# Kernel optimization log

Measured on AMD Instinct MI355X. Metric: run time of the kernel, lower is better.

Reference implementation:

```python
import jax, jax.numpy as jnp
import numpy as np

HEADS = 4
W1 = 7
W2 = 5

def _ln_channel(x, g, b):
    # x: [B,C,H,W]; LayerNorm over channel dim (permute to channel-last)
    xt = x.transpose(0, 2, 3, 1)
    mu = xt.mean(-1, keepdims=True)
    var = xt.var(-1, keepdims=True)
    xt = (xt - mu) / jnp.sqrt(var + 1e-5) * g + b
    return xt.transpose(0, 3, 1, 2)

def _neighborhood_attention(x, qkv_w, qkv_b, proj_w, proj_b, rpb, heads, w):
    # x: [B,C,H,W]; clamped sliding-window (NAT) attention with rel-pos bias
    B, C, H, Wd = x.shape
    hd = C // heads
    xl = x.transpose(0, 2, 3, 1)                      # [B,H,W,C]
    qkv = xl @ qkv_w.T + qkv_b                        # [B,H,W,3C]
    qkv = qkv.reshape(B, H, Wd, 3, heads, hd)
    q = qkv[:, :, :, 0].transpose(0, 3, 1, 2, 4)      # [B,h,H,W,d]
    k = qkv[:, :, :, 1].transpose(0, 3, 1, 2, 4)
    v = qkv[:, :, :, 2].transpose(0, 3, 1, 2, 4)
    q = q * (hd ** -0.5)
    # clamped neighborhood start per row/col
    si = jnp.clip(jnp.arange(H) - w // 2, 0, H - w)   # [H]
    sj = jnp.clip(jnp.arange(Wd) - w // 2, 0, Wd - w) # [W]
    idx_i = si[:, None] + jnp.arange(w)[None, :]      # [H,w]
    idx_j = sj[:, None] + jnp.arange(w)[None, :]      # [W,w]
    # gather neighbor keys/values: [B,h,H,W,w,w,d]
    k_nb = k[:, :, idx_i[:, None, :, None], idx_j[None, :, None, :], :]
    v_nb = v[:, :, idx_i[:, None, :, None], idx_j[None, :, None, :], :]
    attn = jnp.einsum('bnijd,bnijkld->bnijkl', q, k_nb)  # [B,h,H,W,w,w]
    # relative position bias: rel = (w-1) + neighbor_offset - query_offset
    pi = jnp.arange(H) - si                            # [H] in [0,w-1]
    pj = jnp.arange(Wd) - sj
    bi = (w - 1) + jnp.arange(w)[None, :] - pi[:, None]  # [H,w]
    bj = (w - 1) + jnp.arange(w)[None, :] - pj[:, None]  # [W,w]
    bias = rpb[:, bi[:, None, :, None], bj[None, :, None, :]]  # [h,H,W,w,w]
    attn = attn + bias[None]
    attn = jax.nn.softmax(attn.reshape(B, heads, H, Wd, w * w), axis=-1)
    attn = attn.reshape(B, heads, H, Wd, w, w)
    out = jnp.einsum('bnijkl,bnijkld->bnijd', attn, v_nb)  # [B,h,H,W,d]
    out = out.transpose(0, 2, 3, 1, 4).reshape(B, H, Wd, C)
    out = out @ proj_w.T + proj_b
    return out.transpose(0, 3, 1, 2)                   # [B,C,H,W]

def setup_inputs() -> dict:
    key = jax.random.key(0)
    ks = jax.random.split(key, 12)
    B, C, H, W = 2, 128, 56, 56
    s = 0.02
    return {
        'x': jax.random.normal(ks[0], (B, C, H, W), jnp.float32),
        'ln1_g': jnp.ones((C,), jnp.float32),
        'ln1_b': jnp.zeros((C,), jnp.float32),
        'qkv_w1': jax.random.normal(ks[1], (3 * C, C), jnp.float32) * s,
        'qkv_b1': jnp.zeros((3 * C,), jnp.float32),
        'proj_w1': jax.random.normal(ks[2], (C, C), jnp.float32) * s,
        'proj_b1': jnp.zeros((C,), jnp.float32),
        'rpb1': jax.random.normal(ks[3], (HEADS, 2 * W1 - 1, 2 * W1 - 1), jnp.float32) * s,
        'qkv_w2': jax.random.normal(ks[4], (3 * C, C), jnp.float32) * s,
        'qkv_b2': jnp.zeros((3 * C,), jnp.float32),
        'proj_w2': jax.random.normal(ks[5], (C, C), jnp.float32) * s,
        'proj_b2': jnp.zeros((C,), jnp.float32),
        'rpb2': jax.random.normal(ks[6], (HEADS, 2 * W2 - 1, 2 * W2 - 1), jnp.float32) * s,
        'ln2_g': jnp.ones((C,), jnp.float32),
        'ln2_b': jnp.zeros((C,), jnp.float32),
        'fc1_w': jax.random.normal(ks[7], (2 * C, C), jnp.float32) * s,
        'fc1_b': jnp.zeros((2 * C,), jnp.float32),
        'fc2_w': jax.random.normal(ks[8], (C, 2 * C), jnp.float32) * s,
        'fc2_b': jnp.zeros((C,), jnp.float32),
    }

def reference(x, ln1_g, ln1_b, qkv_w1, qkv_b1, proj_w1, proj_b1, rpb1,
              qkv_w2, qkv_b2, proj_w2, proj_b2, rpb2,
              ln2_g, ln2_b, fc1_w, fc1_b, fc2_w, fc2_b):
    xn = _ln_channel(x, ln1_g, ln1_b)
    a = (_neighborhood_attention(xn, qkv_w1, qkv_b1, proj_w1, proj_b1, rpb1, HEADS, W1)
         + _neighborhood_attention(xn, qkv_w2, qkv_b2, proj_w2, proj_b2, rpb2, HEADS, W2))
    x = x + a
    xn2 = _ln_channel(x, ln2_g, ln2_b)
    h = jnp.einsum('bchw,oc->bohw', xn2, fc1_w) + fc1_b[None, :, None, None]
    h = jax.nn.gelu(h, approximate=False)  # torch nn.GELU default = exact erf
    y = jnp.einsum('bchw,oc->bohw', h, fc2_w) + fc2_b[None, :, None, None]
    return x + y
```

## Files before the change

kernel.cpp:

```cpp
#include <hip/hip_runtime.h>
#include <hip/hip_bf16.h>

#define BATCH 2
#define CH    128
#define HH    56
#define WW    56
#define HWS   3136
#define NPOS  6272
#define HEADS 4
#define HD    32

using f32x4 = __attribute__((ext_vector_type(4))) float;
using s16x8 = __attribute__((ext_vector_type(8))) short;

__device__ __forceinline__ unsigned short f2bf(float f) {
  unsigned u = __builtin_bit_cast(unsigned, f);
  u += 0x7FFFu + ((u >> 16) & 1u);
  return (unsigned short)(u >> 16);
}
__device__ __forceinline__ unsigned pack2bf(float a, float b) {
  return (unsigned)f2bf(a) | ((unsigned)f2bf(b) << 16);
}

__global__ __launch_bounds__(256) void convert_weights(
    const float* __restrict__ qw1, const float* __restrict__ qw2,
    const float* __restrict__ pw1, const float* __restrict__ pw2,
    const float* __restrict__ f1w, const float* __restrict__ f2w,
    unsigned short* __restrict__ wb) {
  int bid = blockIdx.x;
  const float* src; unsigned short* dst; int base;
  if (bid < 48)       { src = qw1; dst = wb;           base = bid * 1024; }
  else if (bid < 96)  { src = qw2; dst = wb + 49152;   base = (bid - 48) * 1024; }
  else if (bid < 112) { src = pw1; dst = wb + 98304;   base = (bid - 96) * 1024; }
  else if (bid < 128) { src = pw2; dst = wb + 114688;  base = (bid - 112) * 1024; }
  else if (bid < 160) { src = f1w; dst = wb + 131072;  base = (bid - 128) * 1024; }
  else                { src = f2w; dst = wb + 163840;  base = (bid - 160) * 1024; }
  int i = base + threadIdx.x * 4;
  float4 v = *reinterpret_cast<const float4*>(src + i);
  uint2 o;
  o.x = pack2bf(v.x, v.y);
  o.y = pack2bf(v.z, v.w);
  *reinterpret_cast<uint2*>(dst + i) = o;
}

__global__ __launch_bounds__(256) void ln1_kernel(const float* __restrict__ x,
                                                  const float* __restrict__ g,
                                                  const float* __restrict__ be,
                                                  unsigned short* __restrict__ out) {
  __shared__ float tile[128 * 65];
  __shared__ float mu_s[64];
  __shared__ float rs_s[64];
  const int p0 = blockIdx.x * 64;
  const int b  = (p0 >= HWS) ? 1 : 0;
  const int s0 = p0 - b * HWS;
  const int tid = threadIdx.x;

  for (int idx = tid; idx < 8192; idx += 256) {
    int c = idx >> 6, p = idx & 63;
    tile[c * 65 + p] = x[(size_t)(b * CH + c) * HWS + s0 + p];
  }
  __syncthreads();
  {
    int p = tid >> 2, q = tid & 3;
    float sum = 0.f, sq = 0.f;
#pragma unroll
    for (int t = 0; t < 32; ++t) {
      float v = tile[(q * 32 + t) * 65 + p];
      sum += v; sq += v * v;
    }
    sum += __shfl_xor(sum, 1); sq += __shfl_xor(sq, 1);
    sum += __shfl_xor(sum, 2); sq += __shfl_xor(sq, 2);
    float mu  = sum * 0.0078125f;
    float var = sq * 0.0078125f - mu * mu;
    float rs  = rsqrtf(var + 1e-5f);
    if (q == 0) { mu_s[p] = mu; rs_s[p] = rs; }
  }
  __syncthreads();
  for (int idx = tid; idx < 4096; idx += 256) {
    int nl = idx >> 6, c2 = idx & 63;
    int c0 = 2 * c2;
    float v0 = (tile[c0 * 65 + nl] - mu_s[nl]) * rs_s[nl] * g[c0] + be[c0];
    float v1 = (tile[(c0 + 1) * 65 + nl] - mu_s[nl]) * rs_s[nl] * g[c0 + 1] + be[c0 + 1];
    reinterpret_cast<unsigned*>(out)[(size_t)(p0 + nl) * 64 + c2] = pack2bf(v0, v1);
  }
}

__global__ __launch_bounds__(256) void ln2_kernel(const float* __restrict__ xin,
                                                  const float* __restrict__ g,
                                                  const float* __restrict__ be,
                                                  unsigned short* __restrict__ out) {
  const int tid  = threadIdx.x;
  const int grp  = tid >> 5;
  const int lane = tid & 31;
  const int n = blockIdx.x * 8 + grp;
  const float4* row = reinterpret_cast<const float4*>(xin + (size_t)n * CH);
  float4 v = row[lane];
  float sum = v.x + v.y + v.z + v.w;
  float sq  = v.x * v.x + v.y * v.y + v.z * v.z + v.w * v.w;
#pragma unroll
  for (int o = 1; o < 32; o <<= 1) {
    sum += __shfl_xor(sum, o, 32);
    sq  += __shfl_xor(sq, o, 32);
  }
  float mu = sum * 0.0078125f;
  float rs = rsqrtf(sq * 0.0078125f - mu * mu + 1e-5f);
  float4 gg = reinterpret_cast<const float4*>(g)[lane];
  float4 bb = reinterpret_cast<const float4*>(be)[lane];
  uint2 o2;
  o2.x = pack2bf((v.x - mu) * rs * gg.x + bb.x, (v.y - mu) * rs * gg.y + bb.y);
  o2.y = pack2bf((v.z - mu) * rs * gg.z + bb.z, (v.w - mu) * rs * gg.w + bb.w);
  reinterpret_cast<uint2*>(out + (size_t)n * CH)[lane] = o2;
}

__device__ __forceinline__ void mfma_stage(const unsigned short* __restrict__ A,
                                           const unsigned short* __restrict__ W,
                                           int sA, int sW, int p0, int n0, int kc,
                                           int tid, char* AsB, char* WsB) {
#pragma unroll
  for (int c = 0; c < 2; ++c) {
    int lin = c * 256 + tid;
    int row = lin >> 3;
    int k8  = (lin & 7) << 3;
    int byte = (row << 7) + (k8 << 1);
    byte ^= (row & 7) << 4;
    *reinterpret_cast<uint4*>(AsB + byte) =
        *reinterpret_cast<const uint4*>(A + (size_t)(p0 + row) * sA + kc + k8);
    *reinterpret_cast<uint4*>(WsB + byte) =
        *reinterpret_cast<const uint4*>(W + (size_t)(n0 + row) * sW + kc + k8);
  }
}

__device__ __forceinline__ void mfma_compute(int lane, int wr, int wc,
                                             const char* AsB, const char* WsB,
                                             f32x4 (&acc)[2][2]) {
  const int r_lo = lane & 15, kg = lane >> 4;
#pragma unroll
  for (int ks = 0; ks < 2; ++ks) {
    const int koff = ks * 64 + kg * 16;
    s16x8 a[2], bf[2];
#pragma unroll
    for (int fi = 0; fi < 2; ++fi) {
      int row = wr * 32 + fi * 16 + r_lo;
      int byte = (row << 7) + koff; byte ^= (row & 7) << 4;
      a[fi] = *reinterpret_cast<const s16x8*>(AsB + byte);
    }
#pragma unroll
    for (int ci = 0; ci < 2; ++ci) {
      int row = wc * 32 + ci * 16 + r_lo;
      int byte = (row << 7) + koff; byte ^= (row & 7) << 4;
      bf[ci] = *reinterpret_cast<const s16x8*>(WsB + byte);
    }
#pragma unroll
    for (int fi = 0; fi < 2; ++fi)
#pragma unroll
      for (int ci = 0; ci < 2; ++ci)
        acc[fi][ci] = __builtin_amdgcn_mfma_f32_16x16x32_bf16(a[fi], bf[ci], acc[fi][ci], 0, 0, 0);
  }
}

__device__ __forceinline__ float gelu_exact(float v) {
  return 0.5f * v * (1.0f + erff(v * 0.70710678118654752f));
}

template <int MODE>
__global__ __launch_bounds__(256) void gemm_mfma(const unsigned short* __restrict__ A,
                                                 const unsigned short* __restrict__ W,
                                                 const float* __restrict__ bias,
                                                 void* __restrict__ outv,
                                                 int K, int KOUT) {
  __shared__ char AsB[8192];
  __shared__ char WsB[8192];
  const int tid = threadIdx.x;
  const int lane = tid & 63, w = tid >> 6, wr = w >> 1, wc = w & 1;
  const int p0 = blockIdx.x * 64, n0 = blockIdx.y * 64;
  f32x4 acc[2][2];
#pragma unroll
  for (int i = 0; i < 2; ++i)
#pragma unroll
    for (int j = 0; j < 2; ++j) acc[i][j] = (f32x4){0.f, 0.f, 0.f, 0.f};

  for (int kc = 0; kc < K; kc += 64) {
    if (kc) __syncthreads();
    mfma_stage(A, W, K, K, p0, n0, kc, tid, AsB, WsB);
    __syncthreads();
    mfma_compute(lane, wr, wc, AsB, WsB, acc);
  }
  const int r_lo = lane & 15, kg = lane >> 4;
#pragma unroll
  for (int ci = 0; ci < 2; ++ci) {
    int col = n0 + wc * 32 + ci * 16 + r_lo;
    float bc = bias[col];
#pragma unroll
    for (int fi = 0; fi < 2; ++fi) {
      int row0 = p0 + wr * 32 + fi * 16 + kg * 4;
#pragma unroll
      for (int r = 0; r < 4; ++r) {
        float v = acc[fi][ci][r] + bc;
        if (MODE == 0) {
          reinterpret_cast<float*>(outv)[(size_t)(row0 + r) * KOUT + col] = v;
        } else {
          reinterpret_cast<unsigned short*>(outv)[(size_t)(row0 + r) * KOUT + col] =
              f2bf(gelu_exact(v));
        }
      }
    }
  }
}

__global__ __launch_bounds__(256) void proj_mfma(const unsigned short* __restrict__ A1,
                                                 const unsigned short* __restrict__ W1,
                                                 const float* __restrict__ b1,
                                                 const unsigned short* __restrict__ A2,
                                                 const unsigned short* __restrict__ W2,
                                                 const float* __restrict__ b2,
                                                 const float* __restrict__ xres,
                                                 float* __restrict__ x2out) {
  __shared__ char AsB[8192];
  __shared__ char WsB[8192];
  const int tid = threadIdx.x;
  const int lane = tid & 63, w = tid >> 6, wr = w >> 1, wc = w & 1;
  const int p0 = blockIdx.x * 64, n0 = blockIdx.y * 64;
  const int bb = (p0 >= HWS) ? 1 : 0;
  const int s0 = p0 - bb * HWS;
  f32x4 acc[2][2];
#pragma unroll
  for (int i = 0; i < 2; ++i)
#pragma unroll
    for (int j = 0; j < 2; ++j) acc[i][j] = (f32x4){0.f, 0.f, 0.f, 0.f};

  const unsigned short* Ap[2] = {A1, A2};
  const unsigned short* Wp[2] = {W1, W2};
#pragma unroll
  for (int s2 = 0; s2 < 2; ++s2) {
    for (int kc = 0; kc < 128; kc += 64) {
      if (s2 || kc) __syncthreads();
      mfma_stage(Ap[s2], Wp[s2], 128, 128, p0, n0, kc, tid, AsB, WsB);
      __syncthreads();
      mfma_compute(lane, wr, wc, AsB, WsB, acc);
    }
  }
  const int r_lo = lane & 15, kg = lane >> 4;
#pragma unroll
  for (int ci = 0; ci < 2; ++ci) {
    int col = n0 + wc * 32 + ci * 16 + r_lo;
    float bc = b1[col] + b2[col];
#pragma unroll
    for (int fi = 0; fi < 2; ++fi) {
      int rloc = wr * 32 + fi * 16 + kg * 4;
      float4 xr = *reinterpret_cast<const float4*>(
          &xres[(size_t)(bb * CH + col) * HWS + s0 + rloc]);
      int row0 = p0 + rloc;
      x2out[(size_t)(row0 + 0) * CH + col] = acc[fi][ci][0] + bc + xr.x;
      x2out[(size_t)(row0 + 1) * CH + col] = acc[fi][ci][1] + bc + xr.y;
      x2out[(size_t)(row0 + 2) * CH + col] = acc[fi][ci][2] + bc + xr.z;
      x2out[(size_t)(row0 + 3) * CH + col] = acc[fi][ci][3] + bc + xr.w;
    }
  }
}

__global__ __launch_bounds__(256) void fc2_mfma(const unsigned short* __restrict__ A,
                                                const unsigned short* __restrict__ W,
                                                const float* __restrict__ bias,
                                                const float* __restrict__ x2,
                                                float* __restrict__ out) {
  __shared__ char AsB[8192];
  __shared__ char WsB[8192];
  const int tid = threadIdx.x;
  const int lane = tid & 63, w = tid >> 6, wr = w >> 1, wc = w & 1;
  const int p0 = blockIdx.x * 64, n0 = blockIdx.y * 64;
  const int bb = (p0 >= HWS) ? 1 : 0;
  const int s0 = p0 - bb * HWS;
  f32x4 acc[2][2];
#pragma unroll
  for (int i = 0; i < 2; ++i)
#pragma unroll
    for (int j = 0; j < 2; ++j) acc[i][j] = (f32x4){0.f, 0.f, 0.f, 0.f};

  for (int kc = 0; kc < 256; kc += 64) {
    if (kc) __syncthreads();
    mfma_stage(A, W, 256, 256, p0, n0, kc, tid, AsB, WsB);
    __syncthreads();
    mfma_compute(lane, wr, wc, AsB, WsB, acc);
  }
  const int r_lo = lane & 15, kg = lane >> 4;
#pragma unroll
  for (int ci = 0; ci < 2; ++ci) {
    int col = n0 + wc * 32 + ci * 16 + r_lo;
    float bc = bias[col];
#pragma unroll
    for (int fi = 0; fi < 2; ++fi) {
      int rloc = wr * 32 + fi * 16 + kg * 4;
      int row0 = p0 + rloc;
      float4 o;
      o.x = acc[fi][ci][0] + bc + x2[(size_t)(row0 + 0) * CH + col];
      o.y = acc[fi][ci][1] + bc + x2[(size_t)(row0 + 1) * CH + col];
      o.z = acc[fi][ci][2] + bc + x2[(size_t)(row0 + 2) * CH + col];
      o.w = acc[fi][ci][3] + bc + x2[(size_t)(row0 + 3) * CH + col];
      *reinterpret_cast<float4*>(&out[(size_t)(bb * CH + col) * HWS + s0 + rloc]) = o;
    }
  }
}

template <int NW>
__global__ __launch_bounds__(256) void natten_kernel(const float* __restrict__ qkv,
                                                     const float* __restrict__ rpb,
                                                     unsigned short* __restrict__ out) {
  const int tid = threadIdx.x;
  const int g   = blockIdx.x * 32 + (tid >> 3);
  const int sub = tid & 7;
  const int j  = g % WW;
  const int t1 = g / WW;
  const int i  = t1 % HH;
  const int t2 = t1 / HH;
  const int h  = t2 & 3;
  const int b  = t2 >> 2;
  const int n  = b * HWS + i * WW + j;

  const float scale = 0.17677669529663687f;
  float4 q = *reinterpret_cast<const float4*>(qkv + (size_t)n * 384 + h * 32 + sub * 4);
  q.x *= scale; q.y *= scale; q.z *= scale; q.w *= scale;

  const int si = min(max(i - NW / 2, 0), HH - NW);
  const int sj = min(max(j - NW / 2, 0), WW - NW);
  const float* rb = rpb + h * (2 * NW - 1) * (2 * NW - 1)
                    + (NW - 1 - (i - si)) * (2 * NW - 1) + (NW - 1 - (j - sj));
  float sc[NW * NW];
  float mx = -1e30f;
#pragma unroll
  for (int ki = 0; ki < NW; ++ki) {
#pragma unroll
    for (int kj = 0; kj < NW; ++kj) {
      const int nn = b * HWS + (si + ki) * WW + sj + kj;
      float4 k4 = *reinterpret_cast<const float4*>(qkv + (size_t)nn * 384 + 128 + h * 32 + sub * 4);
      float p = q.x * k4.x + q.y * k4.y + q.z * k4.z + q.w * k4.w;
      p += __shfl_xor(p, 1);
      p += __shfl_xor(p, 2);
      p += __shfl_xor(p, 4);
      p += rb[ki * (2 * NW - 1) + kj];
      sc[ki * NW + kj] = p;
      mx = fmaxf(mx, p);
    }
  }
  float ssum = 0.f;
#pragma unroll
  for (int kk = 0; kk < NW * NW; ++kk) {
    sc[kk] = __expf(sc[kk] - mx);
    ssum += sc[kk];
  }
  float4 o = make_float4(0.f, 0.f, 0.f, 0.f);
#pragma unroll
  for (int ki = 0; ki < NW; ++ki) {
#pragma unroll
    for (int kj = 0; kj < NW; ++kj) {
      const int nn = b * HWS + (si + ki) * WW + sj + kj;
      float4 v4 = *reinterpret_cast<const float4*>(qkv + (size_t)nn * 384 + 256 + h * 32 + sub * 4);
      float p = sc[ki * NW + kj];
      o.x = fmaf(p, v4.x, o.x);
      o.y = fmaf(p, v4.y, o.y);
      o.z = fmaf(p, v4.z, o.z);
      o.w = fmaf(p, v4.w, o.w);
    }
  }
  float inv = 1.0f / ssum;
  uint2 ov;
  ov.x = pack2bf(o.x * inv, o.y * inv);
  ov.y = pack2bf(o.z * inv, o.w * inv);
  *reinterpret_cast<uint2*>(out + (size_t)n * CH + h * 32 + sub * 4) = ov;
}

extern "C" void kernel_launch(void* const* d_in, const int* in_sizes, int n_in,
                              void* d_out, int out_size, void* d_ws, size_t ws_size,
                              hipStream_t stream) {
  const float* x       = (const float*)d_in[0];
  const float* ln1_g   = (const float*)d_in[1];
  const float* ln1_b   = (const float*)d_in[2];
  const float* qkv_w1  = (const float*)d_in[3];
  const float* qkv_b1  = (const float*)d_in[4];
  const float* proj_w1 = (const float*)d_in[5];
  const float* proj_b1 = (const float*)d_in[6];
  const float* rpb1    = (const float*)d_in[7];
  const float* qkv_w2  = (const float*)d_in[8];
  const float* qkv_b2  = (const float*)d_in[9];
  const float* proj_w2 = (const float*)d_in[10];
  const float* proj_b2 = (const float*)d_in[11];
  const float* rpb2    = (const float*)d_in[12];
  const float* ln2_g   = (const float*)d_in[13];
  const float* ln2_b   = (const float*)d_in[14];
  const float* fc1_w   = (const float*)d_in[15];
  const float* fc1_b   = (const float*)d_in[16];
  const float* fc2_w   = (const float*)d_in[17];
  const float* fc2_b   = (const float*)d_in[18];
  float* out = (float*)d_out;

  char* wsb = (char*)d_ws;
  unsigned short* xn    = (unsigned short*)(wsb);
  float*          qkv1  = (float*)(wsb + 1605632);
  float*          qkv2  = (float*)(wsb + 11239424);
  unsigned short* attn1 = (unsigned short*)(wsb + 20873216);
  unsigned short* attn2 = (unsigned short*)(wsb + 22478848);
  float*          x2    = (float*)(wsb + 24084480);
  unsigned short* xn2   = (unsigned short*)(wsb + 27295744);
  unsigned short* hbuf  = (unsigned short*)(wsb + 28901376);
  unsigned short* wbuf  = (unsigned short*)(wsb + 32112640);

  unsigned short* qw1b = wbuf;
  unsigned short* qw2b = wbuf + 49152;
  unsigned short* pw1b = wbuf + 98304;
  unsigned short* pw2b = wbuf + 114688;
  unsigned short* f1wb = wbuf + 131072;
  unsigned short* f2wb = wbuf + 163840;

  convert_weights<<<192, 256, 0, stream>>>(qkv_w1, qkv_w2, proj_w1, proj_w2,
                                           fc1_w, fc2_w, wbuf);
  ln1_kernel<<<98, 256, 0, stream>>>(x, ln1_g, ln1_b, xn);
  gemm_mfma<0><<<dim3(98, 6), 256, 0, stream>>>(xn, qw1b, qkv_b1, qkv1, 128, 384);
  gemm_mfma<0><<<dim3(98, 6), 256, 0, stream>>>(xn, qw2b, qkv_b2, qkv2, 128, 384);
  natten_kernel<7><<<784, 256, 0, stream>>>(qkv1, rpb1, attn1);
  natten_kernel<5><<<784, 256, 0, stream>>>(qkv2, rpb2, attn2);
  proj_mfma<<<dim3(98, 2), 256, 0, stream>>>(attn1, pw1b, proj_b1,
                                             attn2, pw2b, proj_b2, x, x2);
  ln2_kernel<<<784, 256, 0, stream>>>(x2, ln2_g, ln2_b, xn2);
  gemm_mfma<1><<<dim3(98, 4), 256, 0, stream>>>(xn2, f1wb, fc1_b, hbuf, 128, 256);
  fc2_mfma<<<dim3(98, 2), 256, 0, stream>>>(hbuf, f2wb, fc2_b, x2, out);
}
```

Before: 157.8 us.

## Store QKV in bf16, merge QKV/natten launches, fuse LN2 into fc1 GEMM

The QKV projections now write bf16 instead of fp32, which halves the intermediate traffic that the neighborhood-attention gathers read. The two QKV GEMMs become one launch and the two natten kernels become one launch. The LN2 kernel is removed and its normalization is computed inside the fc1 GEMM prologue straight into shared memory. This cuts launches and round trips through global memory, at the cost of bf16 rounding of q/k/v and redundant LN2 work across the four column blocks of fc1.

```diff
diff --git a/kernel.cpp b/kernel.cpp
--- a/kernel.cpp
+++ b/kernel.cpp
@@ -20,6 +20,14 @@
 }
 __device__ __forceinline__ unsigned pack2bf(float a, float b) {
   return (unsigned)f2bf(a) | ((unsigned)f2bf(b) << 16);
+}
+__device__ __forceinline__ float4 bf4tof(uint2 u) {
+  float4 r;
+  r.x = __builtin_bit_cast(float, u.x << 16);
+  r.y = __builtin_bit_cast(float, u.x & 0xFFFF0000u);
+  r.z = __builtin_bit_cast(float, u.y << 16);
+  r.w = __builtin_bit_cast(float, u.y & 0xFFFF0000u);
+  return r;
 }
 
 __global__ __launch_bounds__(256) void convert_weights(
@@ -85,37 +93,9 @@
   }
 }
 
-__global__ __launch_bounds__(256) void ln2_kernel(const float* __restrict__ xin,
-                                                  const float* __restrict__ g,
-                                                  const float* __restrict__ be,
-                                                  unsigned short* __restrict__ out) {
-  const int tid  = threadIdx.x;
-  const int grp  = tid >> 5;
-  const int lane = tid & 31;
-  const int n = blockIdx.x * 8 + grp;
-  const float4* row = reinterpret_cast<const float4*>(xin + (size_t)n * CH);
-  float4 v = row[lane];
-  float sum = v.x + v.y + v.z + v.w;
-  float sq  = v.x * v.x + v.y * v.y + v.z * v.z + v.w * v.w;
-#pragma unroll
-  for (int o = 1; o < 32; o <<= 1) {
-    sum += __shfl_xor(sum, o, 32);
-    sq  += __shfl_xor(sq, o, 32);
-  }
-  float mu = sum * 0.0078125f;
-  float rs = rsqrtf(sq * 0.0078125f - mu * mu + 1e-5f);
-  float4 gg = reinterpret_cast<const float4*>(g)[lane];
-  float4 bb = reinterpret_cast<const float4*>(be)[lane];
-  uint2 o2;
-  o2.x = pack2bf((v.x - mu) * rs * gg.x + bb.x, (v.y - mu) * rs * gg.y + bb.y);
-  o2.y = pack2bf((v.z - mu) * rs * gg.z + bb.z, (v.w - mu) * rs * gg.w + bb.w);
-  reinterpret_cast<uint2*>(out + (size_t)n * CH)[lane] = o2;
-}
-
-__device__ __forceinline__ void mfma_stage(const unsigned short* __restrict__ A,
-                                           const unsigned short* __restrict__ W,
-                                           int sA, int sW, int p0, int n0, int kc,
-                                           int tid, char* AsB, char* WsB) {
+__device__ __forceinline__ void stage64(const unsigned short* __restrict__ src,
+                                        int stride, int row0, int kc,
+                                        int tid, char* dstB) {
 #pragma unroll
   for (int c = 0; c < 2; ++c) {
     int lin = c * 256 + tid;
@@ -123,31 +103,30 @@
     int k8  = (lin & 7) << 3;
     int byte = (row << 7) + (k8 << 1);
     byte ^= (row & 7) << 4;
-    *reinterpret_cast<uint4*>(AsB + byte) =
-        *reinterpret_cast<const uint4*>(A + (size_t)(p0 + row) * sA + kc + k8);
-    *reinterpret_cast<uint4*>(WsB + byte) =
-        *reinterpret_cast<const uint4*>(W + (size_t)(n0 + row) * sW + kc + k8);
-  }
-}
-
-__device__ __forceinline__ void mfma_compute(int lane, int wr, int wc,
-                                             const char* AsB, const char* WsB,
+    *reinterpret_cast<uint4*>(dstB + byte) =
+        *reinterpret_cast<const uint4*>(src + (size_t)(row0 + row) * stride + kc + k8);
+  }
+}
+
+__device__ __forceinline__ void tile_compute(const char* AsB, int aStrideB, int aKoffB,
+                                             const char* WsB, int lane, int wr, int wc,
                                              f32x4 (&acc)[2][2]) {
   const int r_lo = lane & 15, kg = lane >> 4;
 #pragma unroll
   for (int ks = 0; ks < 2; ++ks) {
-    const int koff = ks * 64 + kg * 16;
+    const int koffW = ks * 64 + kg * 16;
+    const int koffA = aKoffB + koffW;
     s16x8 a[2], bf[2];
 #pragma unroll
     for (int fi = 0; fi < 2; ++fi) {
       int row = wr * 32 + fi * 16 + r_lo;
-      int byte = (row << 7) + koff; byte ^= (row & 7) << 4;
+      int byte = row * aStrideB + koffA; byte ^= (row & 7) << 4;
       a[fi] = *reinterpret_cast<const s16x8*>(AsB + byte);
     }
 #pragma unroll
     for (int ci = 0; ci < 2; ++ci) {
       int row = wc * 32 + ci * 16 + r_lo;
-      int byte = (row << 7) + koff; byte ^= (row & 7) << 4;
+      int byte = (row << 7) + koffW; byte ^= (row & 7) << 4;
       bf[ci] = *reinterpret_cast<const s16x8*>(WsB + byte);
     }
 #pragma unroll
@@ -162,28 +141,37 @@
   return 0.5f * v * (1.0f + erff(v * 0.70710678118654752f));
 }
 
-template <int MODE>
-__global__ __launch_bounds__(256) void gemm_mfma(const unsigned short* __restrict__ A,
-                                                 const unsigned short* __restrict__ W,
-                                                 const float* __restrict__ bias,
-                                                 void* __restrict__ outv,
-                                                 int K, int KOUT) {
+__global__ __launch_bounds__(256) void qkv_mfma(const unsigned short* __restrict__ A,
+                                                const unsigned short* __restrict__ W1,
+                                                const float* __restrict__ b1,
+                                                unsigned short* __restrict__ o1,
+                                                const unsigned short* __restrict__ W2,
+                                                const float* __restrict__ b2,
+                                                unsigned short* __restrict__ o2) {
   __shared__ char AsB[8192];
   __shared__ char WsB[8192];
   const int tid = threadIdx.x;
   const int lane = tid & 63, w = tid >> 6, wr = w >> 1, wc = w & 1;
-  const int p0 = blockIdx.x * 64, n0 = blockIdx.y * 64;
+  const int p0 = blockIdx.x * 64;
+  const int yy = blockIdx.y;
+  const bool first = yy < 6;
+  const unsigned short* W = first ? W1 : W2;
+  const float* bias = first ? b1 : b2;
+  unsigned short* outp = first ? o1 : o2;
+  const int n0 = (first ? yy : yy - 6) * 64;
+
   f32x4 acc[2][2];
 #pragma unroll
   for (int i = 0; i < 2; ++i)
 #pragma unroll
     for (int j = 0; j < 2; ++j) acc[i][j] = (f32x4){0.f, 0.f, 0.f, 0.f};
 
-  for (int kc = 0; kc < K; kc += 64) {
+  for (int kc = 0; kc < 128; kc += 64) {
     if (kc) __syncthreads();
-    mfma_stage(A, W, K, K, p0, n0, kc, tid, AsB, WsB);
+    stage64(A, 128, p0, kc, tid, AsB);
+    stage64(W, 128, n0, kc, tid, WsB);
     __syncthreads();
-    mfma_compute(lane, wr, wc, AsB, WsB, acc);
+    tile_compute(AsB, 128, 0, WsB, lane, wr, wc, acc);
   }
   const int r_lo = lane & 15, kg = lane >> 4;
 #pragma unroll
@@ -194,15 +182,8 @@
     for (int fi = 0; fi < 2; ++fi) {
       int row0 = p0 + wr * 32 + fi * 16 + kg * 4;
 #pragma unroll
-      for (int r = 0; r < 4; ++r) {
-        float v = acc[fi][ci][r] + bc;
-        if (MODE == 0) {
-          reinterpret_cast<float*>(outv)[(size_t)(row0 + r) * KOUT + col] = v;
-        } else {
-          reinterpret_cast<unsigned short*>(outv)[(size_t)(row0 + r) * KOUT + col] =
-              f2bf(gelu_exact(v));
-        }
-      }
+      for (int r = 0; r < 4; ++r)
+        outp[(size_t)(row0 + r) * 384 + col] = f2bf(acc[fi][ci][r] + bc);
     }
   }
 }
@@ -234,9 +215,10 @@
   for (int s2 = 0; s2 < 2; ++s2) {
     for (int kc = 0; kc < 128; kc += 64) {
       if (s2 || kc) __syncthreads();
-      mfma_stage(Ap[s2], Wp[s2], 128, 128, p0, n0, kc, tid, AsB, WsB);
+      stage64(Ap[s2], 128, p0, kc, tid, AsB);
+      stage64(Wp[s2], 128, n0, kc, tid, WsB);
       __syncthreads();
-      mfma_compute(lane, wr, wc, AsB, WsB, acc);
+      tile_compute(AsB, 128, 0, WsB, lane, wr, wc, acc);
     }
   }
   const int r_lo = lane & 15, kg = lane >> 4;
@@ -254,6 +236,76 @@
       x2out[(size_t)(row0 + 1) * CH + col] = acc[fi][ci][1] + bc + xr.y;
       x2out[(size_t)(row0 + 2) * CH + col] = acc[fi][ci][2] + bc + xr.z;
       x2out[(size_t)(row0 + 3) * CH + col] = acc[fi][ci][3] + bc + xr.w;
+    }
+  }
+}
+
+__global__ __launch_bounds__(256) void fc1ln_mfma(const float* __restrict__ x2,
+                                                  const float* __restrict__ g,
+                                                  const float* __restrict__ be,
+                                                  const unsigned short* __restrict__ W,
+                                                  const float* __restrict__ bias,
+                                                  unsigned short* __restrict__ out) {
+  __shared__ char AsB[16384];
+  __shared__ char WsB[8192];
+  const int tid = threadIdx.x;
+  const int lane = tid & 63, w = tid >> 6, wr = w >> 1, wc = w & 1;
+  const int p0 = blockIdx.x * 64, n0 = blockIdx.y * 64;
+  {
+    const int p = tid >> 2, q = tid & 3;
+    const float* row = x2 + (size_t)(p0 + p) * CH + q * 32;
+    float4 v[8];
+    float sum = 0.f, sq = 0.f;
+#pragma unroll
+    for (int t = 0; t < 8; ++t) {
+      v[t] = *reinterpret_cast<const float4*>(row + t * 4);
+      sum += v[t].x + v[t].y + v[t].z + v[t].w;
+      sq  += v[t].x * v[t].x + v[t].y * v[t].y + v[t].z * v[t].z + v[t].w * v[t].w;
+    }
+    sum += __shfl_xor(sum, 1); sq += __shfl_xor(sq, 1);
+    sum += __shfl_xor(sum, 2); sq += __shfl_xor(sq, 2);
+    float mu = sum * 0.0078125f;
+    float rs = rsqrtf(sq * 0.0078125f - mu * mu + 1e-5f);
+#pragma unroll
+    for (int t = 0; t < 8; t += 2) {
+      int d0 = q * 32 + t * 4;
+      float4 g0 = *reinterpret_cast<const float4*>(g + d0);
+      float4 g1 = *reinterpret_cast<const float4*>(g + d0 + 4);
+      float4 b0 = *reinterpret_cast<const float4*>(be + d0);
+      float4 b1v = *reinterpret_cast<const float4*>(be + d0 + 4);
+      uint4 o;
+      o.x = pack2bf((v[t].x - mu) * rs * g0.x + b0.x, (v[t].y - mu) * rs * g0.y + b0.y);
+      o.y = pack2bf((v[t].z - mu) * rs * g0.z + b0.z, (v[t].w - mu) * rs * g0.w + b0.w);
+      o.z = pack2bf((v[t+1].x - mu) * rs * g1.x + b1v.x, (v[t+1].y - mu) * rs * g1.y + b1v.y);
+      o.w = pack2bf((v[t+1].z - mu) * rs * g1.z + b1v.z, (v[t+1].w - mu) * rs * g1.w + b1v.w);
+      int byte = p * 256 + q * 64 + (t >> 1) * 16;
+      byte ^= (p & 7) << 4;
+      *reinterpret_cast<uint4*>(AsB + byte) = o;
+    }
+  }
+  f32x4 acc[2][2];
+#pragma unroll
+  for (int i = 0; i < 2; ++i)
+#pragma unroll
+    for (int j = 0; j < 2; ++j) acc[i][j] = (f32x4){0.f, 0.f, 0.f, 0.f};
+
+  for (int kc = 0; kc < 128; kc += 64) {
+    __syncthreads();
+    stage64(W, 128, n0, kc, tid, WsB);
+    __syncthreads();
+    tile_compute(AsB, 256, kc * 2, WsB, lane, wr, wc, acc);
+  }
+  const int r_lo = lane & 15, kg = lane >> 4;
+#pragma unroll
+  for (int ci = 0; ci < 2; ++ci) {
+    int col = n0 + wc * 32 + ci * 16 + r_lo;
+    float bc = bias[col];
+#pragma unroll
+    for (int fi = 0; fi < 2; ++fi) {
+      int row0 = p0 + wr * 32 + fi * 16 + kg * 4;
+#pragma unroll
+      for (int r = 0; r < 4; ++r)
+        out[(size_t)(row0 + r) * 256 + col] = f2bf(gelu_exact(acc[fi][ci][r] + bc));
     }
   }
 }
@@ -278,9 +330,10 @@
 
   for (int kc = 0; kc < 256; kc += 64) {
     if (kc) __syncthreads();
-    mfma_stage(A, W, 256, 256, p0, n0, kc, tid, AsB, WsB);
+    stage64(A, 256, p0, kc, tid, AsB);
+    stage64(W, 256, n0, kc, tid, WsB);
     __syncthreads();
-    mfma_compute(lane, wr, wc, AsB, WsB, acc);
+    tile_compute(AsB, 128, 0, WsB, lane, wr, wc, acc);
   }
   const int r_lo = lane & 15, kg = lane >> 4;
 #pragma unroll
@@ -302,11 +355,11 @@
 }
 
 template <int NW>
-__global__ __launch_bounds__(256) void natten_kernel(const float* __restrict__ qkv,
-                                                     const float* __restrict__ rpb,
-                                                     unsigned short* __restrict__ out) {
-  const int tid = threadIdx.x;
-  const int g   = blockIdx.x * 32 + (tid >> 3);
+__device__ __forceinline__ void natten_body(const unsigned short* __restrict__ qkvb,
+                                            const float* __restrict__ rpb,
+                                            unsigned short* __restrict__ out,
+                                            int blk, int tid) {
+  const int g   = blk * 32 + (tid >> 3);
   const int sub = tid & 7;
   const int j  = g % WW;
   const int t1 = g / WW;
@@ -317,7 +370,7 @@
   const int n  = b * HWS + i * WW + j;
 
   const float scale = 0.17677669529663687f;
-  float4 q = *reinterpret_cast<const float4*>(qkv + (size_t)n * 384 + h * 32 + sub * 4);
+  float4 q = bf4tof(*reinterpret_cast<const uint2*>(qkvb + (size_t)n * 384 + h * 32 + sub * 4));
   q.x *= scale; q.y *= scale; q.z *= scale; q.w *= scale;
 
   const int si = min(max(i - NW / 2, 0), HH - NW);
@@ -331,7 +384,8 @@
 #pragma unroll
     for (int kj = 0; kj < NW; ++kj) {
       const int nn = b * HWS + (si + ki) * WW + sj + kj;
-      float4 k4 = *reinterpret_cast<const float4*>(qkv + (size_t)nn * 384 + 128 + h * 32 + sub * 4);
+      float4 k4 = bf4tof(*reinterpret_cast<const uint2*>(
+          qkvb + (size_t)nn * 384 + 128 + h * 32 + sub * 4));
       float p = q.x * k4.x + q.y * k4.y + q.z * k4.z + q.w * k4.w;
       p += __shfl_xor(p, 1);
       p += __shfl_xor(p, 2);
@@ -353,7 +407,8 @@
 #pragma unroll
     for (int kj = 0; kj < NW; ++kj) {
       const int nn = b * HWS + (si + ki) * WW + sj + kj;
-      float4 v4 = *reinterpret_cast<const float4*>(qkv + (size_t)nn * 384 + 256 + h * 32 + sub * 4);
+      float4 v4 = bf4tof(*reinterpret_cast<const uint2*>(
+          qkvb + (size_t)nn * 384 + 256 + h * 32 + sub * 4));
       float p = sc[ki * NW + kj];
       o.x = fmaf(p, v4.x, o.x);
       o.y = fmaf(p, v4.y, o.y);
@@ -366,6 +421,16 @@
   ov.x = pack2bf(o.x * inv, o.y * inv);
   ov.y = pack2bf(o.z * inv, o.w * inv);
   *reinterpret_cast<uint2*>(out + (size_t)n * CH + h * 32 + sub * 4) = ov;
+}
+
+__global__ __launch_bounds__(256) void natten_fused(const unsigned short* __restrict__ qkv1,
+                                                    const float* __restrict__ rpb1,
+                                                    unsigned short* __restrict__ a1,
+                                                    const unsigned short* __restrict__ qkv2,
+                                                    const float* __restrict__ rpb2,
+                                                    unsigned short* __restrict__ a2) {
+  if (blockIdx.x < 784) natten_body<7>(qkv1, rpb1, a1, blockIdx.x, threadIdx.x);
+  else                  natten_body<5>(qkv2, rpb2, a2, blockIdx.x - 784, threadIdx.x);
 }
 
 extern "C" void kernel_launch(void* const* d_in, const int* in_sizes, int n_in,
@@ -394,14 +459,13 @@
 
   char* wsb = (char*)d_ws;
   unsigned short* xn    = (unsigned short*)(wsb);
-  float*          qkv1  = (float*)(wsb + 1605632);
-  float*          qkv2  = (float*)(wsb + 11239424);
-  unsigned short* attn1 = (unsigned short*)(wsb + 20873216);
-  unsigned short* attn2 = (unsigned short*)(wsb + 22478848);
-  float*          x2    = (float*)(wsb + 24084480);
-  unsigned short* xn2   = (unsigned short*)(wsb + 27295744);
-  unsigned short* hbuf  = (unsigned short*)(wsb + 28901376);
-  unsigned short* wbuf  = (unsigned short*)(wsb + 32112640);
+  unsigned short* qkv1  = (unsigned short*)(wsb + 1605632);
+  unsigned short* qkv2  = (unsigned short*)(wsb + 6422528);
+  unsigned short* attn1 = (unsigned short*)(wsb + 11239424);
+  unsigned short* attn2 = (unsigned short*)(wsb + 12845056);
+  float*          x2    = (float*)(wsb + 14450688);
+  unsigned short* hbuf  = (unsigned short*)(wsb + 17661952);
+  unsigned short* wbuf  = (unsigned short*)(wsb + 20873216);
 
   unsigned short* qw1b = wbuf;
   unsigned short* qw2b = wbuf + 49152;
@@ -413,13 +477,10 @@
   convert_weights<<<192, 256, 0, stream>>>(qkv_w1, qkv_w2, proj_w1, proj_w2,
                                            fc1_w, fc2_w, wbuf);
   ln1_kernel<<<98, 256, 0, stream>>>(x, ln1_g, ln1_b, xn);
-  gemm_mfma<0><<<dim3(98, 6), 256, 0, stream>>>(xn, qw1b, qkv_b1, qkv1, 128, 384);
-  gemm_mfma<0><<<dim3(98, 6), 256, 0, stream>>>(xn, qw2b, qkv_b2, qkv2, 128, 384);
-  natten_kernel<7><<<784, 256, 0, stream>>>(qkv1, rpb1, attn1);
-  natten_kernel<5><<<784, 256, 0, stream>>>(qkv2, rpb2, attn2);
+  qkv_mfma<<<dim3(98, 12), 256, 0, stream>>>(xn, qw1b, qkv_b1, qkv1, qw2b, qkv_b2, qkv2);
+  natten_fused<<<1568, 256, 0, stream>>>(qkv1, rpb1, attn1, qkv2, rpb2, attn2);
   proj_mfma<<<dim3(98, 2), 256, 0, stream>>>(attn1, pw1b, proj_b1,
                                              attn2, pw2b, proj_b2, x, x2);
-  ln2_kernel<<<784, 256, 0, stream>>>(x2, ln2_g, ln2_b, xn2);
-  gemm_mfma<1><<<dim3(98, 4), 256, 0, stream>>>(xn2, f1wb, fc1_b, hbuf, 128, 256);
+  fc1ln_mfma<<<dim3(98, 4), 256, 0, stream>>>(x2, ln2_g, ln2_b, f1wb, fc1_b, hbuf);
   fc2_mfma<<<dim3(98, 2), 256, 0, stream>>>(hbuf, f2wb, fc2_b, x2, out);
 }
```

Measured after the change: 156.3 us. No clear change (-1.0%).
